# Kernel tuning notes

Hardware: AMD Instinct MI355X
Metric: run time of the kernel (lower is better)

## Reference

```python
import jax, jax.numpy as jnp
import numpy as np
import math

HEAD_DIM = 256
NUM_HEADS = 8
NUM_KV_HEADS = 1
ROPE_THETA = 10000.0


def _rope_cos_sin(position_ids, dim, base, dtype):
    # inv_freq: [dim//2]
    inv_freq = 1.0 / (base ** (jnp.arange(0, dim, 2, dtype=jnp.float32) / dim))
    # freqs: [B, S, dim//2]
    freqs = position_ids.astype(jnp.float32)[..., None] * inv_freq[None, None, :]
    emb = jnp.concatenate([freqs, freqs], axis=-1)  # [B, S, dim]
    return jnp.cos(emb).astype(dtype), jnp.sin(emb).astype(dtype)


def _rotate_half(x):
    half = x.shape[-1] // 2
    return jnp.concatenate([-x[..., half:], x[..., :half]], axis=-1)


def setup_inputs() -> dict:
    key = jax.random.key(0)
    ks = jax.random.split(key, 6)
    B, S, H = 2, 2048, 2048
    hidden_states = jax.random.normal(ks[0], (B, S, H), dtype=jnp.float32)
    attention_mask = jnp.zeros((B, 1, S, S), dtype=jnp.float32)
    position_ids = jnp.arange(B * S, dtype=jnp.int64).reshape(B, S) % S
    wq = jax.random.normal(ks[1], (H, NUM_HEADS * HEAD_DIM), dtype=jnp.float32) * 0.02
    wk = jax.random.normal(ks[2], (H, NUM_KV_HEADS * HEAD_DIM), dtype=jnp.float32) * 0.02
    wv = jax.random.normal(ks[3], (H, NUM_KV_HEADS * HEAD_DIM), dtype=jnp.float32) * 0.02
    wo = jax.random.normal(ks[4], (NUM_HEADS * HEAD_DIM, H), dtype=jnp.float32) * 0.02
    return {"hidden_states": hidden_states, "attention_mask": attention_mask,
            "position_ids": position_ids, "wq": wq, "wk": wk, "wv": wv, "wo": wo}


def reference(hidden_states, attention_mask, position_ids, wq, wk, wv, wo):
    B, S, _ = hidden_states.shape
    q = (hidden_states @ wq).reshape(B, S, NUM_HEADS, HEAD_DIM).transpose(0, 2, 1, 3)
    k = (hidden_states @ wk).reshape(B, S, NUM_KV_HEADS, HEAD_DIM).transpose(0, 2, 1, 3)
    v = (hidden_states @ wv).reshape(B, S, NUM_KV_HEADS, HEAD_DIM).transpose(0, 2, 1, 3)

    cos, sin = _rope_cos_sin(position_ids, HEAD_DIM, ROPE_THETA, hidden_states.dtype)
    cos = cos[:, None, :, :]  # [B,1,S,D]
    sin = sin[:, None, :, :]
    q = q * cos + _rotate_half(q) * sin
    k = k * cos + _rotate_half(k) * sin

    # repeat_kv (GQA/MQA expansion)
    n_rep = NUM_HEADS // NUM_KV_HEADS
    k = jnp.repeat(k, n_rep, axis=1)  # [B,H,S,D]
    v = jnp.repeat(v, n_rep, axis=1)

    scores = jnp.einsum('bhqd,bhkd->bhqk', q, k) / math.sqrt(HEAD_DIM)
    scores = scores + attention_mask
    probs = jax.nn.softmax(scores.astype(jnp.float32), axis=-1).astype(q.dtype)
    attn = jnp.einsum('bhqk,bhkd->bhqd', probs, v)  # [B,H,S,D]
    attn = attn.transpose(0, 2, 1, 3).reshape(B, S, NUM_HEADS * HEAD_DIM)
    return attn @ wo
```

## Files before the change

### kernel.cpp

```cpp
#include <hip/hip_runtime.h>
#include <hip/hip_bf16.h>

typedef unsigned short u16;
using f32x4  = __attribute__((ext_vector_type(4))) float;
using bf16x8 = __attribute__((ext_vector_type(8))) __bf16;
using u16x8  = __attribute__((ext_vector_type(8))) unsigned short;
using u16x4  = __attribute__((ext_vector_type(4))) unsigned short;

__device__ __forceinline__ float bf2f(u16 v) {
  union { unsigned u; float f; } x; x.u = ((unsigned)v) << 16; return x.f;
}
__device__ __forceinline__ u16 f2bf(float f) {
  union { float f; unsigned u; } x; x.f = f;
  unsigned r = x.u + 0x7fffu + ((x.u >> 16) & 1u);
  return (u16)(r >> 16);
}
__device__ __forceinline__ void async_load16(const u16* g, u16* l) {
  __builtin_amdgcn_global_load_lds(
      (const __attribute__((address_space(1))) unsigned int*)g,
      (__attribute__((address_space(3))) unsigned int*)l, 16, 0, 0);
}
__device__ __forceinline__ float fexp2(float x) {
#if __has_builtin(__builtin_amdgcn_exp2f)
  return __builtin_amdgcn_exp2f(x);
#else
  return exp2f(x);
#endif
}
__device__ __forceinline__ float vmax4(f32x4 v) {
  return fmaxf(fmaxf(v[0], v[1]), fmaxf(v[2], v[3]));
}
__device__ __forceinline__ int swz_col(int col, int rowk) {
  return (col & ~63) | ((((col >> 3) & 7) ^ rowk) << 3) | (col & 7);
}

__global__ __launch_bounds__(256) void cast_f32_bf16_sw(const float* __restrict__ in,
                                                        u16* __restrict__ out) {
  long i = ((long)blockIdx.x * 256 + threadIdx.x) * 8;
  int m = (int)(i >> 11);
  int col = (int)(i & 2047);
  float4 a = *(const float4*)(in + i);
  float4 b = *(const float4*)(in + i + 4);
  u16x8 v;
  v[0] = f2bf(a.x); v[1] = f2bf(a.y); v[2] = f2bf(a.z); v[3] = f2bf(a.w);
  v[4] = f2bf(b.x); v[5] = f2bf(b.y); v[6] = f2bf(b.z); v[7] = f2bf(b.w);
  *(u16x8*)(out + ((long)m << 11) + swz_col(col, m & 7)) = v;
}

__global__ __launch_bounds__(256) void trans_all(const float* __restrict__ wq,
                                                 const float* __restrict__ wk,
                                                 const float* __restrict__ wv,
                                                 const float* __restrict__ wo,
                                                 u16* __restrict__ wqkvT, u16* __restrict__ woT) {
  const int z = blockIdx.z, bx = blockIdx.x, by = blockIdx.y;
  if (z == 1 && bx >= 64) return;
  const float* src; int srs; u16* dst;
  const int R0 = bx * 32;
  if (z == 0) {
    if (R0 < 2048)      { src = wq + R0;          srs = 2048; }
    else if (R0 < 2304) { src = wk + (R0 - 2048); srs = 256;  }
    else                { src = wv + (R0 - 2304); srs = 256;  }
    dst = wqkvT;
  } else { src = wo + R0; srs = 2048; dst = woT; }
  __shared__ float t[32][33];
  int tx = threadIdx.x, ty = threadIdx.y;
  int br = by * 32;
#pragma unroll
  for (int i = 0; i < 32; i += 8)
    t[ty + i][tx] = src[(long)(br + ty + i) * srs + tx];
  __syncthreads();
#pragma unroll
  for (int i = 0; i < 32; i += 8) {
    int R = R0 + ty + i, C = br + tx;
    dst[(long)R * 2048 + swz_col(C, R & 7)] = f2bf(t[tx][ty + i]);
  }
}

template <typename CT>
__global__ __launch_bounds__(256) void gemm_bt(const u16* __restrict__ A, const u16* __restrict__ Bt,
                                               CT* __restrict__ C, int M, int N, int K) {
  __shared__ __attribute__((aligned(16))) u16 sA[128 * 64];
  __shared__ __attribute__((aligned(16))) u16 sB[128 * 64];
  const int n0 = blockIdx.x * 128, m0 = blockIdx.y * 128;
  const int tid = threadIdx.x;
  const int w = tid >> 6, lane = tid & 63;
  const int l15 = lane & 15, quad = lane >> 4;
  const int wm = (w >> 1) * 64, wn = (w & 1) * 64;
  const int lrow = lane >> 3, lcol = (lane & 7) * 8;
  const u16* Ag = A + (long)(m0 + lrow) * K + lcol;
  const u16* Bg = Bt + (long)(n0 + lrow) * K + lcol;
  const int g0 = ((quad ^ (l15 & 7)) << 3);
  f32x4 acc[4][4] = {};
  for (int k0 = 0; k0 < K; k0 += 64) {
#pragma unroll
    for (int i = 0; i < 4; ++i) {
      int rr = (w * 4 + i) * 8;
      async_load16(Ag + (long)rr * K + k0, &sA[rr * 64]);
      async_load16(Bg + (long)rr * K + k0, &sB[rr * 64]);
    }
    __syncthreads();
#pragma unroll
    for (int kk2 = 0; kk2 < 2; ++kk2) {
      const int go = kk2 ? (g0 ^ 32) : g0;
      bf16x8 af[4], bf[4];
#pragma unroll
      for (int t = 0; t < 4; ++t) {
        af[t] = *(const bf16x8*)&sA[(wm + t * 16 + l15) * 64 + go];
        bf[t] = *(const bf16x8*)&sB[(wn + t * 16 + l15) * 64 + go];
      }
#pragma unroll
      for (int mt = 0; mt < 4; ++mt)
#pragma unroll
        for (int nt = 0; nt < 4; ++nt)
          acc[mt][nt] = __builtin_amdgcn_mfma_f32_16x16x32_bf16(af[mt], bf[nt], acc[mt][nt], 0, 0, 0);
    }
    __syncthreads();
  }
#pragma unroll
  for (int mt = 0; mt < 4; ++mt)
#pragma unroll
    for (int nt = 0; nt < 4; ++nt)
#pragma unroll
      for (int r = 0; r < 4; ++r) {
        long idx = (long)(m0 + wm + mt * 16 + quad * 4 + r) * N + (n0 + wn + nt * 16 + l15);
        if constexpr (sizeof(CT) == 4) C[idx] = acc[mt][nt][r];
        else                           C[idx] = f2bf(acc[mt][nt][r]);
      }
}

__global__ __launch_bounds__(256) void rope_pack(u16* __restrict__ qkv, u16* __restrict__ kp) {
  const int row = blockIdx.x;
  const int tid = threadIdx.x;
  const int d = tid & 127;
  const int s = row & 2047;
  float ang = (float)s * fexp2(-(float)d * 0.10381025296523007f);
  float sn, cs;
  sincosf(ang, &sn, &cs);
  long base = (long)row * 2560;
#pragma unroll
  for (int j = 0; j < 4; ++j) {
    int h = (tid >> 7) + j * 2;
    long p = base + h * 256 + d;
    float x0 = bf2f(qkv[p]), x1 = bf2f(qkv[p + 128]);
    qkv[p]       = f2bf(x0 * cs - x1 * sn);
    qkv[p + 128] = f2bf(x1 * cs + x0 * sn);
  }
  if (tid < 128) {
    long p = base + 2048 + d;
    float x0 = bf2f(qkv[p]), x1 = bf2f(qkv[p + 128]);
    float y0 = x0 * cs - x1 * sn, y1 = x1 * cs + x0 * sn;
    int b = row >> 11, t = (row >> 6) & 31, r = row & 63;
    long sw = (r >> 1) & 7;
    long tb = (long)(b * 32 + t) * 8 * 2048;
#pragma unroll
    for (int u = 0; u < 2; ++u) {
      int D = d + u * 128;
      long off = tb + (long)(D >> 5) * 2048 + r * 32 + (D & 31);
      long off2 = (((off >> 3) ^ sw) << 3) | (off & 7);
      kp[off2] = f2bf(u ? y1 : y0);
    }
  }
}

__global__ __launch_bounds__(256) void pack_vt(const u16* __restrict__ qkv, u16* __restrict__ vp) {
  __shared__ u16 sm[32][40];
  int x = blockIdx.x, y = blockIdx.y, b = blockIdx.z;
  int tx = threadIdx.x, ty = threadIdx.y;
  long inrow = (long)b * 2048 + (y >> 1) * 64 + (y & 1) * 32;
#pragma unroll
  for (int i = 0; i < 32; i += 8)
    sm[ty + i][tx] = qkv[(inrow + ty + i) * 2560 + 2304 + x * 32 + tx];
  __syncthreads();
  long obase = ((long)(b * 32 + (y >> 1)) * 2 + (y & 1)) * 8192 + (long)x * 1024;
#pragma unroll
  for (int i = 0; i < 32; i += 8) {
    long el = obase + (ty + i) * 32 + tx;
    el ^= (long)((((ty + i) >> 1) & 7) << 3);
    vp[el] = sm[tx][ty + i];
  }
}

__global__ __launch_bounds__(256, 1) void flash_attn(const u16* __restrict__ qkv,
                                                     const u16* __restrict__ kp,
                                                     const u16* __restrict__ vp,
                                                     u16* __restrict__ attn) {
  const int qt = blockIdx.x, h = blockIdx.y, b = blockIdx.z;
  const int tid = threadIdx.x, w = tid >> 6, lane = tid & 63;
  const int l15 = lane & 15, quad = lane >> 4;
  __shared__ __attribute__((aligned(16))) u16 sK[2][16384];
  __shared__ __attribute__((aligned(16))) u16 sV[2][16384];
  __shared__ __attribute__((aligned(16))) u16 sP[4][2304];
  const long rowb = (long)b * 2048;
  const int qrow0 = qt * 128 + w * 32;
  const int swz_rd = (l15 >> 1) * 64 + ((((l15 & 1) << 2) | quad) ^ (l15 >> 1)) * 8;

  bf16x8 aqA[8], aqB[8];
  {
    const u16* qpA = qkv + (rowb + qrow0 + l15) * 2560 + h * 256 + quad * 8;
    const u16* qpB = qpA + 16 * 2560;
#pragma unroll
    for (int kk = 0; kk < 8; ++kk) {
      aqA[kk] = *(const bf16x8*)(qpA + kk * 32);
      aqB[kk] = *(const bf16x8*)(qpB + kk * 32);
    }
  }

  float mA = -1e30f, lA = 0.f, mB = -1e30f, lB = 0.f;
  f32x4 accA[16] = {}, accB[16] = {};
  const float SC = 0.09016844005556021f;

  u16* PwA = &sP[w][0];
  u16* PwB = &sP[w][1152];
  const u16* kpb = kp + (long)b * 32 * 16384;
  const u16* vpb = vp + (long)b * 32 * 16384;

#pragma unroll
  for (int j = 0; j < 8; ++j) {
    int base = (w * 8 + j) * 512;
    async_load16(kpb + base + lane * 8, &sK[0][base]);
    async_load16(vpb + base + lane * 8, &sV[0][base]);
  }
  __syncthreads();

  for (int it = 0; it < 32; ++it) {
    const int cur = it & 1;
    const int nx = (it < 31) ? it + 1 : 31;
    const u16* ktn = kpb + (long)nx * 16384;
    const u16* vtn = vpb + (long)nx * 16384;
#pragma unroll
    for (int j = 0; j < 8; ++j) {
      int base = (w * 8 + j) * 512;
      async_load16(ktn + base + lane * 8, &sK[cur ^ 1][base]);
      async_load16(vtn + base + lane * 8, &sV[cur ^ 1][base]);
    }
    f32x4 scA[4] = {}, scB[4] = {};
#pragma unroll
    for (int kk = 0; kk < 8; ++kk)
#pragma unroll
      for (int nt = 0; nt < 4; ++nt) {
        bf16x8 bk = *(const bf16x8*)&sK[cur][kk * 2048 + nt * 512 + swz_rd];
        scA[nt] = __builtin_amdgcn_mfma_f32_16x16x32_bf16(bk, aqA[kk], scA[nt], 0, 0, 0);
        scB[nt] = __builtin_amdgcn_mfma_f32_16x16x32_bf16(bk, aqB[kk], scB[nt], 0, 0, 0);
      }

    {
      float mx = fmaxf(fmaxf(vmax4(scA[0]), vmax4(scA[1])),
                       fmaxf(vmax4(scA[2]), vmax4(scA[3]))) * SC;
      float s1 = __shfl_xor(mx, 16, 64);
      float s2 = __shfl_xor(mx, 32, 64);
      float s3 = __shfl_xor(mx, 48, 64);
      mx = fmaxf(fmaxf(mx, s1), fmaxf(s2, s3));
      if (!__all(mx - mA <= 8.f)) {
        float mnew = fmaxf(mA, mx);
        float al = fexp2(mA - mnew);
        mA = mnew;
        lA *= al;
#pragma unroll
        for (int r = 0; r < 4; ++r) {
          float ar = __shfl(al, quad * 4 + r, 16);
#pragma unroll
          for (int t = 0; t < 16; ++t) accA[t][r] *= ar;
        }
      }
      float rs = 0.f;
#pragma unroll
      for (int nt = 0; nt < 4; ++nt) {
        u16x4 pk;
#pragma unroll
        for (int r = 0; r < 4; ++r) {
          float pv = fexp2(scA[nt][r] * SC - mA);
          rs += pv;
          pk[r] = f2bf(pv);
        }
        *(u16x4*)&PwA[l15 * 72 + nt * 16 + quad * 4] = pk;
      }
      lA += rs;
    }
    asm volatile("s_waitcnt lgkmcnt(0)" ::: "memory");
    bf16x8 paA0 = *(const bf16x8*)&PwA[l15 * 72 + quad * 8];
    bf16x8 paA1 = *(const bf16x8*)&PwA[l15 * 72 + 32 + quad * 8];
    bf16x8 bv0[16];
#pragma unroll
    for (int t = 0; t < 16; ++t) {
      bv0[t] = *(const bf16x8*)&sV[cur][t * 512 + swz_rd];
      accA[t] = __builtin_amdgcn_mfma_f32_16x16x32_bf16(paA0, bv0[t], accA[t], 0, 0, 0);
    }
    {
      float mx = fmaxf(fmaxf(vmax4(scB[0]), vmax4(scB[1])),
                       fmaxf(vmax4(scB[2]), vmax4(scB[3]))) * SC;
      float s1 = __shfl_xor(mx, 16, 64);
      float s2 = __shfl_xor(mx, 32, 64);
      float s3 = __shfl_xor(mx, 48, 64);
      mx = fmaxf(fmaxf(mx, s1), fmaxf(s2, s3));
      if (!__all(mx - mB <= 8.f)) {
        float mnew = fmaxf(mB, mx);
        float al = fexp2(mB - mnew);
        mB = mnew;
        lB *= al;
#pragma unroll
        for (int r = 0; r < 4; ++r) {
          float ar = __shfl(al, quad * 4 + r, 16);
#pragma unroll
          for (int t = 0; t < 16; ++t) accB[t][r] *= ar;
        }
      }
      float rs = 0.f;
#pragma unroll
      for (int nt = 0; nt < 4; ++nt) {
        u16x4 pk;
#pragma unroll
        for (int r = 0; r < 4; ++r) {
          float pv = fexp2(scB[nt][r] * SC - mB);
          rs += pv;
          pk[r] = f2bf(pv);
        }
        *(u16x4*)&PwB[l15 * 72 + nt * 16 + quad * 4] = pk;
      }
      lB += rs;
    }
    asm volatile("s_waitcnt lgkmcnt(0)" ::: "memory");
    bf16x8 paB0 = *(const bf16x8*)&PwB[l15 * 72 + quad * 8];
    bf16x8 paB1 = *(const bf16x8*)&PwB[l15 * 72 + 32 + quad * 8];
#pragma unroll
    for (int t = 0; t < 16; ++t) {
      accB[t] = __builtin_amdgcn_mfma_f32_16x16x32_bf16(paB0, bv0[t], accB[t], 0, 0, 0);
      bf16x8 bv1 = *(const bf16x8*)&sV[cur][8192 + t * 512 + swz_rd];
      accA[t] = __builtin_amdgcn_mfma_f32_16x16x32_bf16(paA1, bv1, accA[t], 0, 0, 0);
      accB[t] = __builtin_amdgcn_mfma_f32_16x16x32_bf16(paB1, bv1, accB[t], 0, 0, 0);
    }
    __syncthreads();
  }
  {
    float t1 = __shfl_xor(lA, 16, 64);
    float t2 = __shfl_xor(lA, 32, 64);
    float t3 = __shfl_xor(lA, 48, 64);
    lA = (lA + t1) + (t2 + t3);
    t1 = __shfl_xor(lB, 16, 64);
    t2 = __shfl_xor(lB, 32, 64);
    t3 = __shfl_xor(lB, 48, 64);
    lB = (lB + t1) + (t2 + t3);
  }
#pragma unroll
  for (int r = 0; r < 4; ++r) {
    float lrA = __shfl(lA, quad * 4 + r, 16);
    float lrB = __shfl(lB, quad * 4 + r, 16);
    float rinvA = 1.f / lrA;
    float rinvB = 1.f / lrB;
    int key = (quad * 4 + r) & 7;
#pragma unroll
    for (int t = 0; t < 16; ++t) {
      int col = h * 256 + t * 16 + l15;
      int sc_ = swz_col(col, key);
      attn[(rowb + qrow0 + quad * 4 + r) * 2048 + sc_]      = f2bf(accA[t][r] * rinvA);
      attn[(rowb + qrow0 + 16 + quad * 4 + r) * 2048 + sc_] = f2bf(accB[t][r] * rinvB);
    }
  }
}

extern "C" void kernel_launch(void* const* d_in, const int* in_sizes, int n_in,
                              void* d_out, int out_size, void* d_ws, size_t ws_size,
                              hipStream_t stream) {
  const float* hidden = (const float*)d_in[0];
  const float* wq = (const float*)d_in[3];
  const float* wk = (const float*)d_in[4];
  const float* wv = (const float*)d_in[5];
  const float* wo = (const float*)d_in[6];
  float* out = (float*)d_out;

  char* ws = (char*)d_ws;
  u16* QKV   = (u16*)(ws);
  u16* WqkvT = (u16*)(ws + 20971520);
  u16* Kp    = (u16*)(ws + 20971520);
  u16* Vp    = (u16*)(ws + 23068672);
  u16* WoT   = (u16*)(ws + 31457280);
  u16* HB    = (u16*)(ws + 39845888);
  u16* ATT   = (u16*)(ws + 39845888);

  cast_f32_bf16_sw<<<4096, 256, 0, stream>>>(hidden, HB);
  trans_all<<<dim3(80, 64, 2), dim3(32, 8), 0, stream>>>(wq, wk, wv, wo, WqkvT, WoT);

  gemm_bt<u16><<<dim3(20, 32), dim3(256), 0, stream>>>(HB, WqkvT, QKV, 4096, 2560, 2048);

  rope_pack<<<4096, 256, 0, stream>>>(QKV, Kp);
  pack_vt<<<dim3(8, 64, 2), dim3(32, 8), 0, stream>>>(QKV, Vp);

  flash_attn<<<dim3(16, 8, 2), dim3(256), 0, stream>>>(QKV, Kp, Vp, ATT);

  gemm_bt<float><<<dim3(16, 32), dim3(256), 0, stream>>>(ATT, WoT, out, 4096, 2048, 2048);
}
```

Before: 370.4 us.

## Split KV sequence across two wave groups per block with LDS merge in flash attention

Doubles the flash attention block to 512 threads: two groups of four waves each process half of the key/value sequence for the same 128 query rows, using 32-key half tiles. At the end, group 1 spills its partial accumulators and max/sum statistics to shared memory and group 0 merges them with a log-sum-exp rescale before writing. The aim is more waves per CU to hide latency and more parallelism over the fixed 256-block grid. In exchange it adds a merge pass, shared-memory reuse for the scratch buffer, halves per-iteration MFMA work relative to synchronisation, and the launch bound of (512,2) may force register spills.

```diff
diff --git a/kernel.cpp b/kernel.cpp
--- a/kernel.cpp
+++ b/kernel.cpp
@@ -180,18 +180,20 @@
   }
 }
 
-__global__ __launch_bounds__(256, 1) void flash_attn(const u16* __restrict__ qkv,
+__global__ __launch_bounds__(512, 2) void flash_attn(const u16* __restrict__ qkv,
                                                      const u16* __restrict__ kp,
                                                      const u16* __restrict__ vp,
                                                      u16* __restrict__ attn) {
   const int qt = blockIdx.x, h = blockIdx.y, b = blockIdx.z;
   const int tid = threadIdx.x, w = tid >> 6, lane = tid & 63;
   const int l15 = lane & 15, quad = lane >> 4;
-  __shared__ __attribute__((aligned(16))) u16 sK[2][16384];
-  __shared__ __attribute__((aligned(16))) u16 sV[2][16384];
-  __shared__ __attribute__((aligned(16))) u16 sP[4][2304];
+  const int g = w >> 2, wq = w & 3;
+  __shared__ __attribute__((aligned(16))) u16 S[75776];
+  u16* sKg = &S[g * 16384];
+  u16* sVg = &S[32768 + g * 16384];
+  u16* Pw  = &S[65536 + w * 1280];
   const long rowb = (long)b * 2048;
-  const int qrow0 = qt * 128 + w * 32;
+  const int qrow0 = qt * 128 + wq * 32;
   const int swz_rd = (l15 >> 1) * 64 + ((((l15 & 1) << 2) | quad) ^ (l15 >> 1)) * 8;
 
   bf16x8 aqA[8], aqB[8];
@@ -209,43 +211,43 @@
   f32x4 accA[16] = {}, accB[16] = {};
   const float SC = 0.09016844005556021f;
 
-  u16* PwA = &sP[w][0];
-  u16* PwB = &sP[w][1152];
-  const u16* kpb = kp + (long)b * 32 * 16384;
-  const u16* vpb = vp + (long)b * 32 * 16384;
-
-#pragma unroll
-  for (int j = 0; j < 8; ++j) {
-    int base = (w * 8 + j) * 512;
-    async_load16(kpb + base + lane * 8, &sK[0][base]);
-    async_load16(vpb + base + lane * 8, &sV[0][base]);
-  }
+  const u16* kpg = kp + ((long)b * 32 + g * 16) * 16384;
+  const u16* vpg = vp + ((long)b * 32 + g * 16) * 16384;
+
+  const auto stage = [&](int ht, int bf) {
+    const int T = ht >> 1, hf = ht & 1;
+#pragma unroll
+    for (int j = 0; j < 8; ++j) {
+      int idx = wq * 8 + j;
+      if (idx < 16) {
+        int c = idx >> 1, part = idx & 1;
+        async_load16(kpg + (long)T * 16384 + c * 2048 + hf * 1024 + part * 512 + lane * 8,
+                     sKg + bf * 8192 + c * 1024 + part * 512);
+      } else {
+        int o = (idx - 16) * 512;
+        async_load16(vpg + (long)T * 16384 + hf * 8192 + o + lane * 8,
+                     sVg + bf * 8192 + o);
+      }
+    }
+  };
+
+  stage(0, 0);
   __syncthreads();
 
-  for (int it = 0; it < 32; ++it) {
-    const int cur = it & 1;
-    const int nx = (it < 31) ? it + 1 : 31;
-    const u16* ktn = kpb + (long)nx * 16384;
-    const u16* vtn = vpb + (long)nx * 16384;
-#pragma unroll
-    for (int j = 0; j < 8; ++j) {
-      int base = (w * 8 + j) * 512;
-      async_load16(ktn + base + lane * 8, &sK[cur ^ 1][base]);
-      async_load16(vtn + base + lane * 8, &sV[cur ^ 1][base]);
-    }
-    f32x4 scA[4] = {}, scB[4] = {};
+  for (int ht = 0; ht < 32; ++ht) {
+    const int cur = ht & 1;
+    stage(ht < 31 ? ht + 1 : 31, cur ^ 1);
+    f32x4 scA[2] = {}, scB[2] = {};
 #pragma unroll
     for (int kk = 0; kk < 8; ++kk)
 #pragma unroll
-      for (int nt = 0; nt < 4; ++nt) {
-        bf16x8 bk = *(const bf16x8*)&sK[cur][kk * 2048 + nt * 512 + swz_rd];
+      for (int nt = 0; nt < 2; ++nt) {
+        bf16x8 bk = *(const bf16x8*)&sKg[cur * 8192 + kk * 1024 + nt * 512 + swz_rd];
         scA[nt] = __builtin_amdgcn_mfma_f32_16x16x32_bf16(bk, aqA[kk], scA[nt], 0, 0, 0);
         scB[nt] = __builtin_amdgcn_mfma_f32_16x16x32_bf16(bk, aqB[kk], scB[nt], 0, 0, 0);
       }
-
     {
-      float mx = fmaxf(fmaxf(vmax4(scA[0]), vmax4(scA[1])),
-                       fmaxf(vmax4(scA[2]), vmax4(scA[3]))) * SC;
+      float mx = fmaxf(vmax4(scA[0]), vmax4(scA[1])) * SC;
       float s1 = __shfl_xor(mx, 16, 64);
       float s2 = __shfl_xor(mx, 32, 64);
       float s3 = __shfl_xor(mx, 48, 64);
@@ -253,8 +255,7 @@
       if (!__all(mx - mA <= 8.f)) {
         float mnew = fmaxf(mA, mx);
         float al = fexp2(mA - mnew);
-        mA = mnew;
-        lA *= al;
+        mA = mnew; lA *= al;
 #pragma unroll
         for (int r = 0; r < 4; ++r) {
           float ar = __shfl(al, quad * 4 + r, 16);
@@ -264,30 +265,19 @@
       }
       float rs = 0.f;
 #pragma unroll
-      for (int nt = 0; nt < 4; ++nt) {
+      for (int nt = 0; nt < 2; ++nt) {
         u16x4 pk;
 #pragma unroll
         for (int r = 0; r < 4; ++r) {
           float pv = fexp2(scA[nt][r] * SC - mA);
-          rs += pv;
-          pk[r] = f2bf(pv);
+          rs += pv; pk[r] = f2bf(pv);
         }
-        *(u16x4*)&PwA[l15 * 72 + nt * 16 + quad * 4] = pk;
+        *(u16x4*)&Pw[l15 * 40 + nt * 16 + quad * 4] = pk;
       }
       lA += rs;
     }
-    asm volatile("s_waitcnt lgkmcnt(0)" ::: "memory");
-    bf16x8 paA0 = *(const bf16x8*)&PwA[l15 * 72 + quad * 8];
-    bf16x8 paA1 = *(const bf16x8*)&PwA[l15 * 72 + 32 + quad * 8];
-    bf16x8 bv0[16];
-#pragma unroll
-    for (int t = 0; t < 16; ++t) {
-      bv0[t] = *(const bf16x8*)&sV[cur][t * 512 + swz_rd];
-      accA[t] = __builtin_amdgcn_mfma_f32_16x16x32_bf16(paA0, bv0[t], accA[t], 0, 0, 0);
-    }
     {
-      float mx = fmaxf(fmaxf(vmax4(scB[0]), vmax4(scB[1])),
-                       fmaxf(vmax4(scB[2]), vmax4(scB[3]))) * SC;
+      float mx = fmaxf(vmax4(scB[0]), vmax4(scB[1])) * SC;
       float s1 = __shfl_xor(mx, 16, 64);
       float s2 = __shfl_xor(mx, 32, 64);
       float s3 = __shfl_xor(mx, 48, 64);
@@ -295,8 +285,7 @@
       if (!__all(mx - mB <= 8.f)) {
         float mnew = fmaxf(mB, mx);
         float al = fexp2(mB - mnew);
-        mB = mnew;
-        lB *= al;
+        mB = mnew; lB *= al;
 #pragma unroll
         for (int r = 0; r < 4; ++r) {
           float ar = __shfl(al, quad * 4 + r, 16);
@@ -306,53 +295,76 @@
       }
       float rs = 0.f;
 #pragma unroll
-      for (int nt = 0; nt < 4; ++nt) {
+      for (int nt = 0; nt < 2; ++nt) {
         u16x4 pk;
 #pragma unroll
         for (int r = 0; r < 4; ++r) {
           float pv = fexp2(scB[nt][r] * SC - mB);
-          rs += pv;
-          pk[r] = f2bf(pv);
+          rs += pv; pk[r] = f2bf(pv);
         }
-        *(u16x4*)&PwB[l15 * 72 + nt * 16 + quad * 4] = pk;
+        *(u16x4*)&Pw[640 + l15 * 40 + nt * 16 + quad * 4] = pk;
       }
       lB += rs;
     }
     asm volatile("s_waitcnt lgkmcnt(0)" ::: "memory");
-    bf16x8 paB0 = *(const bf16x8*)&PwB[l15 * 72 + quad * 8];
-    bf16x8 paB1 = *(const bf16x8*)&PwB[l15 * 72 + 32 + quad * 8];
+    bf16x8 paA = *(const bf16x8*)&Pw[l15 * 40 + quad * 8];
+    bf16x8 paB = *(const bf16x8*)&Pw[640 + l15 * 40 + quad * 8];
 #pragma unroll
     for (int t = 0; t < 16; ++t) {
-      accB[t] = __builtin_amdgcn_mfma_f32_16x16x32_bf16(paB0, bv0[t], accB[t], 0, 0, 0);
-      bf16x8 bv1 = *(const bf16x8*)&sV[cur][8192 + t * 512 + swz_rd];
-      accA[t] = __builtin_amdgcn_mfma_f32_16x16x32_bf16(paA1, bv1, accA[t], 0, 0, 0);
-      accB[t] = __builtin_amdgcn_mfma_f32_16x16x32_bf16(paB1, bv1, accB[t], 0, 0, 0);
+      bf16x8 bv = *(const bf16x8*)&sVg[cur * 8192 + t * 512 + swz_rd];
+      accA[t] = __builtin_amdgcn_mfma_f32_16x16x32_bf16(paA, bv, accA[t], 0, 0, 0);
+      accB[t] = __builtin_amdgcn_mfma_f32_16x16x32_bf16(paB, bv, accB[t], 0, 0, 0);
     }
     __syncthreads();
   }
   {
-    float t1 = __shfl_xor(lA, 16, 64);
-    float t2 = __shfl_xor(lA, 32, 64);
-    float t3 = __shfl_xor(lA, 48, 64);
+    float t1 = __shfl_xor(lA, 16, 64), t2 = __shfl_xor(lA, 32, 64), t3 = __shfl_xor(lA, 48, 64);
     lA = (lA + t1) + (t2 + t3);
-    t1 = __shfl_xor(lB, 16, 64);
-    t2 = __shfl_xor(lB, 32, 64);
-    t3 = __shfl_xor(lB, 48, 64);
+    t1 = __shfl_xor(lB, 16, 64); t2 = __shfl_xor(lB, 32, 64); t3 = __shfl_xor(lB, 48, 64);
     lB = (lB + t1) + (t2 + t3);
   }
-#pragma unroll
-  for (int r = 0; r < 4; ++r) {
-    float lrA = __shfl(lA, quad * 4 + r, 16);
-    float lrB = __shfl(lB, quad * 4 + r, 16);
-    float rinvA = 1.f / lrA;
-    float rinvB = 1.f / lrB;
-    int key = (quad * 4 + r) & 7;
+  float* scr = (float*)S;
+  float* mlb = scr + 36864;
+  if (g == 1) {
+    float* sc0 = scr + wq * 9216;
 #pragma unroll
     for (int t = 0; t < 16; ++t) {
-      int col = h * 256 + t * 16 + l15;
-      int sc_ = swz_col(col, key);
-      attn[(rowb + qrow0 + quad * 4 + r) * 2048 + sc_]      = f2bf(accA[t][r] * rinvA);
-      attn[(rowb + qrow0 + 16 + quad * 4 + r) * 2048 + sc_] = f2bf(accB[t][r] * rinvB);
+      *(f32x4*)&sc0[(t * 16 + l15) * 36 + quad * 4]      = accA[t];
+      *(f32x4*)&sc0[(t * 16 + l15) * 36 + 16 + quad * 4] = accB[t];
+    }
+    if (quad == 0) {
+      mlb[wq * 64 + l15]      = mA;
+      mlb[wq * 64 + 16 + l15] = lA;
+      mlb[wq * 64 + 32 + l15] = mB;
+      mlb[wq * 64 + 48 + l15] = lB;
+    }
+  }
+  __syncthreads();
+  if (g == 0) {
+    const float* sc0 = scr + wq * 9216;
+#pragma unroll
+    for (int s = 0; s < 2; ++s) {
+      float m0 = s ? mB : mA, l0 = s ? lB : lA;
+      float m1 = mlb[wq * 64 + s * 32 + l15];
+      float l1 = mlb[wq * 64 + s * 32 + 16 + l15];
+      float ms = fmaxf(m0, m1);
+      float f0 = fexp2(m0 - ms), f1 = fexp2(m1 - ms);
+      float li = 1.f / (f0 * l0 + f1 * l1);
+      float g0 = f0 * li, g1 = f1 * li;
+#pragma unroll
+      for (int t = 0; t < 16; ++t) {
+        f32x4 oth = *(const f32x4*)&sc0[(t * 16 + l15) * 36 + s * 16 + quad * 4];
+        f32x4 mine = s ? accB[t] : accA[t];
+        int col = h * 256 + t * 16 + l15;
+#pragma unroll
+        for (int r = 0; r < 4; ++r) {
+          float g0r = __shfl(g0, quad * 4 + r, 16);
+          float g1r = __shfl(g1, quad * 4 + r, 16);
+          int row = qrow0 + s * 16 + quad * 4 + r;
+          attn[(rowb + row) * 2048 + swz_col(col, row & 7)] =
+              f2bf(g0r * mine[r] + g1r * oth[r]);
+        }
+      }
     }
   }
 }
@@ -384,7 +396,7 @@
   rope_pack<<<4096, 256, 0, stream>>>(QKV, Kp);
   pack_vt<<<dim3(8, 64, 2), dim3(32, 8), 0, stream>>>(QKV, Vp);
 
-  flash_attn<<<dim3(16, 8, 2), dim3(256), 0, stream>>>(QKV, Kp, Vp, ATT);
+  flash_attn<<<dim3(16, 8, 2), dim3(512), 0, stream>>>(QKV, Kp, Vp, ATT);
 
   gemm_bt<float><<<dim3(16, 32), dim3(256), 0, stream>>>(ATT, WoT, out, 4096, 2048, 2048);
 }
```

Result: slower. 393.3 us (+6.2%).
